# Kernel tuning notes

Hardware: AMD Instinct MI355X
Metric: run time of the kernel (lower is better)

The kernel has to match this reference:

```python
import jax, jax.numpy as jnp
import numpy as np

B, S, DIN = 16, 960, 7
HID, HEADS, LAYERS = 512, 8, 4
PERIODS = (24, 48, 96)
OUT_LEN = 96
HEAD_DIM = HID // HEADS
FFN = 4 * HID


def setup_inputs() -> dict:
    key = jax.random.key(0)
    ks = jax.random.split(key, 20)
    sc = 0.02
    return {
        "x": jax.random.normal(ks[0], (B, S, DIN), dtype=jnp.float32),
        "input_proj_w": jax.random.normal(ks[1], (HID, DIN), dtype=jnp.float32) * sc,
        "input_proj_b": jnp.zeros((HID,), dtype=jnp.float32),
        "in_proj_w": jax.random.normal(ks[2], (LAYERS, 3 * HID, HID), dtype=jnp.float32) * sc,
        "in_proj_b": jnp.zeros((LAYERS, 3 * HID), dtype=jnp.float32),
        "out_proj_w": jax.random.normal(ks[3], (LAYERS, HID, HID), dtype=jnp.float32) * sc,
        "out_proj_b": jnp.zeros((LAYERS, HID), dtype=jnp.float32),
        "ffn_w1": jax.random.normal(ks[4], (LAYERS, FFN, HID), dtype=jnp.float32) * sc,
        "ffn_b1": jnp.zeros((LAYERS, FFN), dtype=jnp.float32),
        "ffn_w2": jax.random.normal(ks[5], (LAYERS, HID, FFN), dtype=jnp.float32) * sc,
        "ffn_b2": jnp.zeros((LAYERS, HID), dtype=jnp.float32),
        "ln1_w": jnp.ones((LAYERS, HID), dtype=jnp.float32),
        "ln1_b": jnp.zeros((LAYERS, HID), dtype=jnp.float32),
        "ln2_w": jnp.ones((LAYERS, HID), dtype=jnp.float32),
        "ln2_b": jnp.zeros((LAYERS, HID), dtype=jnp.float32),
        "output_proj_w": jax.random.normal(ks[6], (1, HID), dtype=jnp.float32) * sc,
        "output_proj_b": jnp.zeros((1,), dtype=jnp.float32),
    }


def _layer_norm(x, w, b, eps=1e-5):
    mu = jnp.mean(x, axis=-1, keepdims=True)
    var = jnp.mean(jnp.square(x - mu), axis=-1, keepdims=True)
    return (x - mu) * jax.lax.rsqrt(var + eps) * w + b


def _mha(x, wqkv, bqkv, wo, bo):
    # x: [N, P, H]; self-attention, PyTorch nn.MultiheadAttention math (eval mode)
    N, P, _ = x.shape
    qkv = x @ wqkv.T + bqkv                      # [N, P, 3H]
    q, k, v = jnp.split(qkv, 3, axis=-1)
    q = q.reshape(N, P, HEADS, HEAD_DIM)
    k = k.reshape(N, P, HEADS, HEAD_DIM)
    v = v.reshape(N, P, HEADS, HEAD_DIM)
    scores = jnp.einsum("nqhd,nkhd->nhqk", q, k) / jnp.sqrt(jnp.float32(HEAD_DIM))
    attn = jax.nn.softmax(scores, axis=-1)
    out = jnp.einsum("nhqk,nkhd->nqhd", attn, v).reshape(N, P, HID)
    return out @ wo.T + bo


def _times_block(x, period, wqkv, bqkv, wo, bo, w1, b1, w2, b2, g1, be1, g2, be2):
    # x: [B, S, H], S % period == 0. Batch all period slices together
    # (replaces the original Python loop over num_periods).
    Bc, Sc, H = x.shape
    xb = x.reshape(Bc * (Sc // period), period, H)
    attn = _mha(xb, wqkv, bqkv, wo, bo)
    xb = _layer_norm(xb + attn, g1, be1)
    ffn = jax.nn.gelu(xb @ w1.T + b1, approximate=False) @ w2.T + b2
    xb = _layer_norm(xb + ffn, g2, be2)
    return xb.reshape(Bc, Sc, H)


def reference(x, input_proj_w, input_proj_b, in_proj_w, in_proj_b, out_proj_w,
              out_proj_b, ffn_w1, ffn_b1, ffn_w2, ffn_b2, ln1_w, ln1_b,
              ln2_w, ln2_b, output_proj_w, output_proj_b):
    h = x @ input_proj_w.T + input_proj_b        # [B, S, H]
    branches = []
    for period in PERIODS:
        ph = h
        for l in range(LAYERS):
            ph = _times_block(ph, period,
                              in_proj_w[l], in_proj_b[l], out_proj_w[l], out_proj_b[l],
                              ffn_w1[l], ffn_b1[l], ffn_w2[l], ffn_b2[l],
                              ln1_w[l], ln1_b[l], ln2_w[l], ln2_b[l])
        branches.append(ph)
    h = jnp.mean(jnp.stack(branches, axis=0), axis=0)     # [B, S, H]
    out = h @ output_proj_w.T + output_proj_b             # [B, S, 1]
    # AdaptiveAvgPool1d(OUT_LEN) with S % OUT_LEN == 0 -> uniform block mean
    out = out.reshape(B, OUT_LEN, S // OUT_LEN, 1).mean(axis=2)  # [B, OUT_LEN, 1]
    return out
```

## Files before the change

### kernel.cpp

```cpp
#include <hip/hip_runtime.h>
#include <hip/hip_bf16.h>

typedef __bf16 bf16;
typedef __attribute__((ext_vector_type(8))) __bf16 bf16x8;
typedef __attribute__((ext_vector_type(4))) __bf16 bf16x4;
typedef __attribute__((ext_vector_type(4))) float f32x4;

#define TOKENS 15360
#define HID    512
#define FFN_D  2048
#define QKV_D  1536

__device__ __forceinline__ float gelu_erf(float x) {
  const float z = fabsf(x) * 0.70710678118654752f;
#if __has_builtin(__builtin_amdgcn_rcpf)
  const float t = __builtin_amdgcn_rcpf(fmaf(0.3275911f, z, 1.f));
#else
  const float t = 1.f / fmaf(0.3275911f, z, 1.f);
#endif
  float p = fmaf(1.061405429f, t, -1.453152027f);
  p = fmaf(p, t, 1.421413741f);
  p = fmaf(p, t, -0.284496736f);
  p = fmaf(p, t, 0.254829592f);
  p *= t;
  const float e  = __expf(-z * z);
  const float er = fmaf(-p, e, 1.f);
  return 0.5f * x * (1.f + copysignf(er, x));
}

__global__ __launch_bounds__(256) void cvt_kernel(const float* __restrict__ src,
                                                  bf16* __restrict__ dst, int n4) {
  const int i = (blockIdx.x * 256 + threadIdx.x);
  if (i >= n4) return;
  const float4 v = ((const float4*)src)[i];
  bf16x4 d = {(bf16)v.x, (bf16)v.y, (bf16)v.z, (bf16)v.w};
  *(bf16x4*)(dst + (size_t)i * 4) = d;
}

__global__ __launch_bounds__(256) void cvt_w2_kernel(const float* __restrict__ src,
                                                     bf16* __restrict__ dst, int n4) {
  const int i = (blockIdx.x * 256 + threadIdx.x);
  if (i >= n4) return;
  const int f  = i * 4;
  const int ln = f >> 11;
  const int c2 = f & 2047;
  const int h  = c2 >> 10;
  const int c  = c2 & 1023;
  const int l  = ln >> 9;
  const int n  = ln & 511;
  const float4 v = ((const float4*)src)[i];
  bf16x4 d = {(bf16)v.x, (bf16)v.y, (bf16)v.z, (bf16)v.w};
  *(bf16x4*)(dst + ((((size_t)(l * 2 + h) * 512 + n) << 10) + c)) = d;
}

#define EPI_BIAS_BF16     0
#define EPI_BIAS_RES_BF16 1
#define EPI_BIAS_GELU     2
#define EPI_RES_BF16      3

template <int EPI>
__global__ __launch_bounds__(256) void gemm_bt(
    const bf16* __restrict__ A, const bf16* __restrict__ W,
    const float* __restrict__ bias, const bf16* __restrict__ R,
    bf16* __restrict__ out, int M, int N, int K) {
  __shared__ __align__(16) bf16 As[2 * 128 * 64];
  __shared__ __align__(16) bf16 Bs[2 * 128 * 64];

  const int tid  = threadIdx.x;
  const int lane = tid & 63;
  const int wv   = tid >> 6;
  const int li   = lane & 15;
  const int qd   = lane >> 4;
  const int mw   = (wv & 1) << 6;
  const int nw   = (wv >> 1) << 6;

  const int NB  = gridDim.x;
  const int nwg = NB * gridDim.y;
  int lid = blockIdx.y * NB + blockIdx.x;
  if ((nwg & 7) == 0) lid = (lid & 7) * (nwg >> 3) + (lid >> 3);
  const int n0 = (lid % NB) << 7;
  const int m0 = (lid / NB) << 7;

  f32x4 acc[4][4];
#pragma unroll
  for (int i = 0; i < 4; ++i)
#pragma unroll
    for (int j = 0; j < 4; ++j) acc[i][j] = (f32x4){0.f, 0.f, 0.f, 0.f};

  const bf16* pa[4];
  const bf16* pb[4];
  int off[4];
#pragma unroll
  for (int it = 0; it < 4; ++it) {
    const int fc   = it * 256 + tid;
    const int r    = fc >> 3;
    const int c    = fc & 7;
    const int koff = (c ^ (r & 7)) << 3;
    pa[it]  = A + (size_t)(m0 + r) * K + koff;
    pb[it]  = W + (size_t)(n0 + r) * K + koff;
    off[it] = (it * 256 + (tid & 192)) * 8;
  }

  auto stage = [&](int buf) {
#pragma unroll
    for (int it = 0; it < 4; ++it) {
      __builtin_amdgcn_global_load_lds(
          (const __attribute__((address_space(1))) unsigned int*)pa[it],
          (__attribute__((address_space(3))) unsigned int*)(As + buf * 8192 + off[it]),
          16, 0, 0);
      pa[it] += 64;
    }
#pragma unroll
    for (int it = 0; it < 4; ++it) {
      __builtin_amdgcn_global_load_lds(
          (const __attribute__((address_space(1))) unsigned int*)pb[it],
          (__attribute__((address_space(3))) unsigned int*)(Bs + buf * 8192 + off[it]),
          16, 0, 0);
      pb[it] += 64;
    }
  };

  auto compute = [&](int buf) {
    const bf16* Ab = As + buf * 8192;
    const bf16* Bb = Bs + buf * 8192;
#pragma unroll
    for (int ks = 0; ks < 2; ++ks) {
      const int ck = (ks << 2) + qd;
      bf16x8 af[4], bfv[4];
#pragma unroll
      for (int i = 0; i < 4; ++i) {
        const int mr = mw + i * 16 + li;
        af[i] = *(const bf16x8*)(Ab + mr * 64 + ((ck ^ (li & 7)) << 3));
      }
#pragma unroll
      for (int j = 0; j < 4; ++j) {
        const int nr = nw + j * 16 + li;
        bfv[j] = *(const bf16x8*)(Bb + nr * 64 + ((ck ^ (li & 7)) << 3));
      }
#pragma unroll
      for (int i = 0; i < 4; ++i)
#pragma unroll
        for (int j = 0; j < 4; ++j)
          acc[i][j] = __builtin_amdgcn_mfma_f32_16x16x32_bf16(af[i], bfv[j],
                                                              acc[i][j], 0, 0, 0);
    }
  };

  stage(0);
  int cur = 0;
  for (int k0 = 0; k0 < K - 64; k0 += 64) {
    stage(cur ^ 1);
    asm volatile("s_waitcnt vmcnt(8)" ::: "memory");
    __builtin_amdgcn_s_barrier();
    asm volatile("" ::: "memory");
    compute(cur);
    asm volatile("" ::: "memory");
    __builtin_amdgcn_s_barrier();
    asm volatile("" ::: "memory");
    cur ^= 1;
  }
  asm volatile("s_waitcnt vmcnt(0)" ::: "memory");
  __builtin_amdgcn_s_barrier();
  asm volatile("" ::: "memory");
  compute(cur);

#pragma unroll
  for (int i = 0; i < 4; ++i) {
    const int mrow = m0 + mw + i * 16 + qd * 4;
#pragma unroll
    for (int j = 0; j < 4; ++j) {
      const int ncol = n0 + nw + j * 16 + li;
      float bv = 0.f;
      if (EPI != EPI_RES_BF16) bv = bias[ncol];
#pragma unroll
      for (int r = 0; r < 4; ++r) {
        const size_t off2 = (size_t)(mrow + r) * N + ncol;
        float v = acc[i][j][r] + bv;
        if (EPI == EPI_BIAS_RES_BF16 || EPI == EPI_RES_BF16) v += (float)R[off2];
        out[off2] = (EPI == EPI_BIAS_GELU) ? (bf16)gelu_erf(v) : (bf16)v;
      }
    }
  }
}

template <int P>
__global__ __launch_bounds__(256) void attn_kernel(const bf16* __restrict__ qkv,
                                                   bf16* __restrict__ out) {
  constexpr int PP   = ((P + 15) / 16) * 16;
  constexpr int PK   = ((PP + 31) / 32) * 32;
  constexpr int MT   = PP / 16;
  constexpr int SSTR = PP + 2;
  constexpr int VSTR = PK + 8;
  constexpr int PSTR = PK + 8;
  constexpr int G    = (P * 8 <= 256) ? 8 : ((P * 4 <= 256) ? 4 : 2);

  __shared__ __align__(16) bf16 QK[2 * PP * 64];
  __shared__ __align__(16) bf16 Vt[64 * VSTR];
  __shared__ __align__(16) float Sm[PP * SSTR];
  __shared__ float rsum[PP];

  bf16* Qs = QK;
  bf16* Ks = QK + PP * 64;
  bf16* Ps = QK;

  const int tid  = threadIdx.x;
  const int lane = tid & 63;
  const int wv   = tid >> 6;
  const int li   = lane & 15;
  const int qd   = lane >> 4;
  const int n    = blockIdx.x >> 3;
  const int h    = blockIdx.x & 7;
  const bf16* base = qkv + (size_t)n * P * QKV_D + h * 64;

  for (int t = tid; t < P * 8; t += 256) {
    const int r = t >> 3, c = t & 7;
    const bf16x8 qv = *(const bf16x8*)(base + (size_t)r * QKV_D + c * 8);
    const bf16x8 kv = *(const bf16x8*)(base + (size_t)r * QKV_D + 512 + c * 8);
    *(bf16x8*)(Qs + r * 64 + ((c ^ (r & 7)) * 8)) = qv;
    *(bf16x8*)(Ks + r * 64 + ((c ^ (r & 7)) * 8)) = kv;
  }
  for (int t = tid; t < P * 8; t += 256) {
    const int j = t % P, dc = t / P;
    const bf16x8 vv = *(const bf16x8*)(base + (size_t)j * QKV_D + 1024 + dc * 8);
#pragma unroll
    for (int u = 0; u < 8; ++u) Vt[(dc * 8 + u) * VSTR + j] = vv[u];
  }
  if constexpr (PK > P) {
    for (int t = tid; t < 64 * (PK - P); t += 256) {
      const int d = t / (PK - P), j = P + t % (PK - P);
      Vt[d * VSTR + j] = (bf16)0.f;
    }
  }
  __syncthreads();

  for (int t = wv; t < MT * MT; t += 4) {
    const int ti = t / MT, tj = t % MT;
    f32x4 acc = (f32x4){0.f, 0.f, 0.f, 0.f};
#pragma unroll
    for (int ks = 0; ks < 2; ++ks) {
      const int ck = ks * 4 + qd;
      const int ar = ti * 16 + li;
      const int br = tj * 16 + li;
      const bf16x8 af = *(const bf16x8*)(Qs + ar * 64 + ((ck ^ (ar & 7)) * 8));
      const bf16x8 bv = *(const bf16x8*)(Ks + br * 64 + ((ck ^ (br & 7)) * 8));
      acc = __builtin_amdgcn_mfma_f32_16x16x32_bf16(af, bv, acc, 0, 0, 0);
    }
#pragma unroll
    for (int r = 0; r < 4; ++r)
      Sm[(ti * 16 + qd * 4 + r) * SSTR + tj * 16 + li] = acc[r];
  }
  __syncthreads();

  if (tid < P * G) {
    const int row = tid / G, g = tid % G;
    const float* srow = Sm + row * SSTR;
    bf16* prow = Ps + row * PSTR;
    float mx = -1e30f;
    for (int j = g; j < P; j += G) mx = fmaxf(mx, srow[j]);
#pragma unroll
    for (int m = G >> 1; m; m >>= 1) mx = fmaxf(mx, __shfl_xor(mx, m, 64));
    mx *= 0.125f;
    float sum = 0.f;
    for (int j = g; j < P; j += G) {
      const float e = __expf(srow[j] * 0.125f - mx);
      sum += e;
      prow[j] = (bf16)e;
    }
#pragma unroll
    for (int m = G >> 1; m; m >>= 1) sum += __shfl_xor(sum, m, 64);
    for (int j = P + g; j < PK; j += G) prow[j] = (bf16)0.f;
    if (g == 0) rsum[row] = 1.f / sum;
  }
  __syncthreads();

  for (int t = wv; t < MT * 4; t += 4) {
    const int ti = t >> 2, td = t & 3;
    f32x4 acc = (f32x4){0.f, 0.f, 0.f, 0.f};
#pragma unroll
    for (int ks = 0; ks < PK / 32; ++ks) {
      const int ck = ks * 4 + qd;
      const bf16x8 af = *(const bf16x8*)(Ps + (ti * 16 + li) * PSTR + ck * 8);
      const bf16x8 bv = *(const bf16x8*)(Vt + (td * 16 + li) * VSTR + ck * 8);
      acc = __builtin_amdgcn_mfma_f32_16x16x32_bf16(af, bv, acc, 0, 0, 0);
    }
#pragma unroll
    for (int r = 0; r < 4; ++r) {
      const int row = ti * 16 + qd * 4 + r;
      if (row < P)
        out[(size_t)(n * P + row) * HID + h * 64 + td * 16 + li] =
            (bf16)(acc[r] * rsum[row]);
    }
  }
}

__global__ __launch_bounds__(256) void ln_kernel(const bf16* __restrict__ Y,
                                                 const float* __restrict__ w,
                                                 const float* __restrict__ b,
                                                 bf16* __restrict__ X) {
  const int row  = blockIdx.x * 4 + (threadIdx.x >> 6);
  const int lane = threadIdx.x & 63;
  const bf16x8 yv = *(const bf16x8*)(Y + (size_t)row * HID + 8 * lane);
  float y[8];
#pragma unroll
  for (int u = 0; u < 8; ++u) y[u] = (float)yv[u];
  float s = 0.f, s2 = 0.f;
#pragma unroll
  for (int u = 0; u < 8; ++u) { s += y[u]; s2 += y[u] * y[u]; }
#pragma unroll
  for (int off = 32; off > 0; off >>= 1) {
    s  += __shfl_xor(s, off, 64);
    s2 += __shfl_xor(s2, off, 64);
  }
  const float mean = s * (1.f / 512.f);
  const float var  = s2 * (1.f / 512.f) - mean * mean;
  const float rstd = rsqrtf(var + 1e-5f);
  const float4 w0 = ((const float4*)w)[2 * lane];
  const float4 w1 = ((const float4*)w)[2 * lane + 1];
  const float4 b0 = ((const float4*)b)[2 * lane];
  const float4 b1 = ((const float4*)b)[2 * lane + 1];
  const float wr[8] = {w0.x, w0.y, w0.z, w0.w, w1.x, w1.y, w1.z, w1.w};
  const float br[8] = {b0.x, b0.y, b0.z, b0.w, b1.x, b1.y, b1.z, b1.w};
  bf16x8 o;
#pragma unroll
  for (int u = 0; u < 8; ++u) o[u] = (bf16)((y[u] - mean) * rstd * wr[u] + br[u]);
  *(bf16x8*)(X + (size_t)row * HID + 8 * lane) = o;
}

__global__ __launch_bounds__(256) void inproj_kernel(const float* __restrict__ x,
                                                     const float* __restrict__ w,
                                                     const float* __restrict__ b,
                                                     bf16* __restrict__ h,
                                                     int nbr) {
  const int idx = blockIdx.x * 256 + threadIdx.x;
  const int r = idx >> 9, o = idx & 511;
  float s = b[o];
#pragma unroll
  for (int k = 0; k < 7; ++k) s += x[r * 7 + k] * w[o * 7 + k];
  const bf16 bv = (bf16)s;
  for (int q = 0; q < nbr; ++q) h[idx + (size_t)q * TOKENS * HID] = bv;
}

__global__ __launch_bounds__(256) void outdot_kernel(const bf16* __restrict__ X,
                                                     const float* __restrict__ w,
                                                     float* __restrict__ acc,
                                                     int first) {
  const int row  = blockIdx.x * 4 + (threadIdx.x >> 6);
  const int lane = threadIdx.x & 63;
  const bf16* xr = X + (size_t)row * HID;
  const bf16x8 xa = *(const bf16x8*)(xr + 8 * lane);
  const float4 wa = ((const float4*)w)[2 * lane];
  const float4 wb = ((const float4*)w)[2 * lane + 1];
  float s = (float)xa[0] * wa.x + (float)xa[1] * wa.y + (float)xa[2] * wa.z +
            (float)xa[3] * wa.w + (float)xa[4] * wb.x + (float)xa[5] * wb.y +
            (float)xa[6] * wb.z + (float)xa[7] * wb.w;
#pragma unroll
  for (int off = 32; off > 0; off >>= 1) s += __shfl_xor(s, off, 64);
  if (lane == 0) acc[row] = first ? s : (acc[row] + s);
}

__global__ __launch_bounds__(256) void pool_kernel(const float* __restrict__ acc,
                                                   const float* __restrict__ ob,
                                                   float* __restrict__ out) {
  const int idx = blockIdx.x * 256 + threadIdx.x;
  if (idx >= 16 * 96) return;
  const int bb = idx / 96, o = idx % 96;
  float s = 0.f;
#pragma unroll
  for (int j = 0; j < 10; ++j) s += acc[bb * 960 + o * 10 + j];
  out[idx] = s * (1.f / 30.f) + ob[0];
}

extern "C" void kernel_launch(void* const* d_in, const int* in_sizes, int n_in,
                              void* d_out, int out_size, void* d_ws,
                              size_t ws_size, hipStream_t stream) {
  const float* x          = (const float*)d_in[0];
  const float* ip_w       = (const float*)d_in[1];
  const float* ip_b       = (const float*)d_in[2];
  const float* in_proj_w  = (const float*)d_in[3];
  const float* in_proj_b  = (const float*)d_in[4];
  const float* out_proj_w = (const float*)d_in[5];
  const float* out_proj_b = (const float*)d_in[6];
  const float* ffn_w1     = (const float*)d_in[7];
  const float* ffn_b1     = (const float*)d_in[8];
  const float* ffn_w2     = (const float*)d_in[9];
  const float* ffn_b2     = (const float*)d_in[10];
  const float* ln1_w      = (const float*)d_in[11];
  const float* ln1_b      = (const float*)d_in[12];
  const float* ln2_w      = (const float*)d_in[13];
  const float* ln2_b      = (const float*)d_in[14];
  const float* op_w       = (const float*)d_in[15];
  const float* op_b       = (const float*)d_in[16];

  char* p = (char*)d_ws;
  bf16* Wq  = (bf16*)p; p += (size_t)4 * QKV_D * HID * 2;
  bf16* Wo  = (bf16*)p; p += (size_t)4 * HID * HID * 2;
  bf16* W1  = (bf16*)p; p += (size_t)4 * FFN_D * HID * 2;
  bf16* W2s = (bf16*)p; p += (size_t)4 * HID * FFN_D * 2;
  float* ACC = (float*)p; p += (size_t)TOKENS * 4;
  const size_t remain = ws_size - (size_t)(p - (char*)d_ws);

  const size_t T3 = 3 * (size_t)TOKENS;
  const size_t need_batched = T3 * HID * 2 + T3 * (size_t)FFN_D * 2;
  const size_t need_seq =
      (size_t)TOKENS * HID * 2 + (size_t)TOKENS * FFN_D * 2;
  const bool batched = remain >= need_batched;
  if (!batched && remain < need_seq) return;

  {
    const int nq = 4 * QKV_D * HID / 4, no = 4 * HID * HID / 4,
              n1 = 4 * FFN_D * HID / 4, n2 = 4 * HID * FFN_D / 4;
    cvt_kernel<<<(nq + 255) / 256, 256, 0, stream>>>(in_proj_w, Wq, nq);
    cvt_kernel<<<(no + 255) / 256, 256, 0, stream>>>(out_proj_w, Wo, no);
    cvt_kernel<<<(n1 + 255) / 256, 256, 0, stream>>>(ffn_w1, W1, n1);
    cvt_w2_kernel<<<(n2 + 255) / 256, 256, 0, stream>>>(ffn_w2, W2s, n2);
  }

  static const int periods[3] = {24, 48, 96};
  auto launch_attn = [&](int P, const bf16* q, bf16* o) {
    const int nblk = (TOKENS / P) * 8;
    if (P == 24)      attn_kernel<24><<<nblk, 256, 0, stream>>>(q, o);
    else if (P == 48) attn_kernel<48><<<nblk, 256, 0, stream>>>(q, o);
    else              attn_kernel<96><<<nblk, 256, 0, stream>>>(q, o);
  };

  auto run_layer = [&](int l, int M, bf16* X, bf16* QKV, bf16* ATT, bf16* YB,
                       bf16* H, bool all_br, int br) {
    const int MB = M / 128;
    gemm_bt<EPI_BIAS_BF16><<<dim3(QKV_D / 128, MB), 256, 0, stream>>>(
        X, Wq + (size_t)l * QKV_D * HID, in_proj_b + l * QKV_D, nullptr,
        QKV, M, QKV_D, HID);
    if (all_br) {
      for (int b2 = 0; b2 < 3; ++b2)
        launch_attn(periods[b2], QKV + (size_t)b2 * TOKENS * QKV_D,
                    ATT + (size_t)b2 * TOKENS * HID);
    } else {
      launch_attn(periods[br], QKV, ATT);
    }
    gemm_bt<EPI_BIAS_RES_BF16><<<dim3(HID / 128, MB), 256, 0, stream>>>(
        ATT, Wo + (size_t)l * HID * HID, out_proj_b + l * HID, X, YB,
        M, HID, HID);
    ln_kernel<<<M / 4, 256, 0, stream>>>(YB, ln1_w + l * HID, ln1_b + l * HID, X);
    gemm_bt<EPI_BIAS_GELU><<<dim3(1024 / 128, MB), 256, 0, stream>>>(
        X, W1 + (size_t)l * FFN_D * HID, ffn_b1 + l * FFN_D, nullptr,
        H, M, 1024, HID);
    gemm_bt<EPI_BIAS_RES_BF16><<<dim3(HID / 128, MB), 256, 0, stream>>>(
        H, W2s + (size_t)(l * 2 + 0) * HID * 1024, ffn_b2 + l * HID, X, YB,
        M, HID, 1024);
    gemm_bt<EPI_BIAS_GELU><<<dim3(1024 / 128, MB), 256, 0, stream>>>(
        X, W1 + (size_t)l * FFN_D * HID + (size_t)1024 * HID,
        ffn_b1 + l * FFN_D + 1024, nullptr, H, M, 1024, HID);
    gemm_bt<EPI_RES_BF16><<<dim3(HID / 128, MB), 256, 0, stream>>>(
        H, W2s + (size_t)(l * 2 + 1) * HID * 1024, nullptr, YB, YB,
        M, HID, 1024);
    ln_kernel<<<M / 4, 256, 0, stream>>>(YB, ln2_w + l * HID, ln2_b + l * HID, X);
  };

  if (batched) {
    bf16* X   = (bf16*)p; p += T3 * HID * 2;
    bf16* BUF = (bf16*)p;
    bf16* QKV = BUF;
    bf16* ATT = BUF + T3 * QKV_D;
    bf16* H   = BUF;
    bf16* YB  = BUF + T3 * 1024;
    const int M = (int)T3;

    inproj_kernel<<<TOKENS * HID / 256, 256, 0, stream>>>(x, ip_w, ip_b, X, 3);
    for (int l = 0; l < 4; ++l)
      run_layer(l, M, X, QKV, ATT, YB, H, true, 0);
    for (int br = 0; br < 3; ++br)
      outdot_kernel<<<TOKENS / 4, 256, 0, stream>>>(
          X + (size_t)br * TOKENS * HID, op_w, ACC, br == 0);
  } else {
    bf16* X   = (bf16*)p; p += (size_t)TOKENS * HID * 2;
    bf16* SCR = (bf16*)p; p += (size_t)TOKENS * FFN_D * 2;
    bf16* QKV = SCR;
    bf16* ATT = SCR + (size_t)TOKENS * QKV_D;
    bf16* H   = SCR;
    bf16* YB  = SCR + (size_t)TOKENS * 1024;
    const int M = TOKENS;

    for (int br = 0; br < 3; ++br) {
      inproj_kernel<<<TOKENS * HID / 256, 256, 0, stream>>>(x, ip_w, ip_b, X, 1);
      for (int l = 0; l < 4; ++l)
        run_layer(l, M, X, QKV, ATT, YB, H, false, br);
      outdot_kernel<<<TOKENS / 4, 256, 0, stream>>>(X, op_w, ACC, br == 0);
    }
  }
  pool_kernel<<<6, 256, 0, stream>>>(ACC, op_b, (float*)d_out);
}
```

Before: 2.203 ms.

## Share layer-0 QKV across branches and unsplit FFN when workspace allows

At layer 0 all three period branches start from the same input projection, so the QKV GEMM now runs once on TOKENS rows and every branch's attention reads that shared result. When the workspace is large enough, the FFN becomes one full-width GELU GEMM and one K=2048 down-projection. This replaces the two half-width pairs, removing extra launches and a residual round-trip through YB. The unsplit path needs a separate YB buffer and so more workspace. It also converts W2 without the split layout.

```diff
diff --git a/kernel.cpp b/kernel.cpp
--- a/kernel.cpp
+++ b/kernel.cpp
@@ -392,18 +392,19 @@
   const float* op_b       = (const float*)d_in[16];
 
   char* p = (char*)d_ws;
-  bf16* Wq  = (bf16*)p; p += (size_t)4 * QKV_D * HID * 2;
-  bf16* Wo  = (bf16*)p; p += (size_t)4 * HID * HID * 2;
-  bf16* W1  = (bf16*)p; p += (size_t)4 * FFN_D * HID * 2;
-  bf16* W2s = (bf16*)p; p += (size_t)4 * HID * FFN_D * 2;
+  bf16* Wq = (bf16*)p; p += (size_t)4 * QKV_D * HID * 2;
+  bf16* Wo = (bf16*)p; p += (size_t)4 * HID * HID * 2;
+  bf16* W1 = (bf16*)p; p += (size_t)4 * FFN_D * HID * 2;
+  bf16* W2 = (bf16*)p; p += (size_t)4 * HID * FFN_D * 2;
   float* ACC = (float*)p; p += (size_t)TOKENS * 4;
   const size_t remain = ws_size - (size_t)(p - (char*)d_ws);
 
   const size_t T3 = 3 * (size_t)TOKENS;
-  const size_t need_batched = T3 * HID * 2 + T3 * (size_t)FFN_D * 2;
-  const size_t need_seq =
-      (size_t)TOKENS * HID * 2 + (size_t)TOKENS * FFN_D * 2;
-  const bool batched = remain >= need_batched;
+  const size_t need_unsplit = T3 * HID * 2 + T3 * (size_t)FFN_D * 2 + T3 * HID * 2;
+  const size_t need_split   = T3 * HID * 2 + T3 * (size_t)FFN_D * 2;
+  const size_t need_seq     = (size_t)TOKENS * HID * 2 + (size_t)TOKENS * FFN_D * 2;
+  const bool unsplit = remain >= need_unsplit;
+  const bool batched = remain >= need_split;
   if (!batched && remain < need_seq) return;
 
   {
@@ -412,7 +413,10 @@
     cvt_kernel<<<(nq + 255) / 256, 256, 0, stream>>>(in_proj_w, Wq, nq);
     cvt_kernel<<<(no + 255) / 256, 256, 0, stream>>>(out_proj_w, Wo, no);
     cvt_kernel<<<(n1 + 255) / 256, 256, 0, stream>>>(ffn_w1, W1, n1);
-    cvt_w2_kernel<<<(n2 + 255) / 256, 256, 0, stream>>>(ffn_w2, W2s, n2);
+    if (unsplit)
+      cvt_kernel<<<(n2 + 255) / 256, 256, 0, stream>>>(ffn_w2, W2, n2);
+    else
+      cvt_w2_kernel<<<(n2 + 255) / 256, 256, 0, stream>>>(ffn_w2, W2, n2);
   }
 
   static const int periods[3] = {24, 48, 96};
@@ -423,16 +427,17 @@
     else              attn_kernel<96><<<nblk, 256, 0, stream>>>(q, o);
   };
 
-  auto run_layer = [&](int l, int M, bf16* X, bf16* QKV, bf16* ATT, bf16* YB,
-                       bf16* H, bool all_br, int br) {
+  auto run_layer = [&](int l, int M, int qkvM, bf16* X, bf16* QKV, bf16* ATT,
+                       bf16* YB, bf16* H, bool all_br, int br, bool unspl) {
     const int MB = M / 128;
-    gemm_bt<EPI_BIAS_BF16><<<dim3(QKV_D / 128, MB), 256, 0, stream>>>(
+    gemm_bt<EPI_BIAS_BF16><<<dim3(QKV_D / 128, qkvM / 128), 256, 0, stream>>>(
         X, Wq + (size_t)l * QKV_D * HID, in_proj_b + l * QKV_D, nullptr,
-        QKV, M, QKV_D, HID);
+        QKV, qkvM, QKV_D, HID);
     if (all_br) {
-      for (int b2 = 0; b2 < 3; ++b2)
-        launch_attn(periods[b2], QKV + (size_t)b2 * TOKENS * QKV_D,
-                    ATT + (size_t)b2 * TOKENS * HID);
+      for (int b2 = 0; b2 < 3; ++b2) {
+        const bf16* q = QKV + (qkvM == M ? (size_t)b2 * TOKENS * QKV_D : 0);
+        launch_attn(periods[b2], q, ATT + (size_t)b2 * TOKENS * HID);
+      }
     } else {
       launch_attn(periods[br], QKV, ATT);
     }
@@ -440,33 +445,48 @@
         ATT, Wo + (size_t)l * HID * HID, out_proj_b + l * HID, X, YB,
         M, HID, HID);
     ln_kernel<<<M / 4, 256, 0, stream>>>(YB, ln1_w + l * HID, ln1_b + l * HID, X);
-    gemm_bt<EPI_BIAS_GELU><<<dim3(1024 / 128, MB), 256, 0, stream>>>(
-        X, W1 + (size_t)l * FFN_D * HID, ffn_b1 + l * FFN_D, nullptr,
-        H, M, 1024, HID);
-    gemm_bt<EPI_BIAS_RES_BF16><<<dim3(HID / 128, MB), 256, 0, stream>>>(
-        H, W2s + (size_t)(l * 2 + 0) * HID * 1024, ffn_b2 + l * HID, X, YB,
-        M, HID, 1024);
-    gemm_bt<EPI_BIAS_GELU><<<dim3(1024 / 128, MB), 256, 0, stream>>>(
-        X, W1 + (size_t)l * FFN_D * HID + (size_t)1024 * HID,
-        ffn_b1 + l * FFN_D + 1024, nullptr, H, M, 1024, HID);
-    gemm_bt<EPI_RES_BF16><<<dim3(HID / 128, MB), 256, 0, stream>>>(
-        H, W2s + (size_t)(l * 2 + 1) * HID * 1024, nullptr, YB, YB,
-        M, HID, 1024);
+    if (unspl) {
+      gemm_bt<EPI_BIAS_GELU><<<dim3(FFN_D / 128, MB), 256, 0, stream>>>(
+          X, W1 + (size_t)l * FFN_D * HID, ffn_b1 + l * FFN_D, nullptr,
+          H, M, FFN_D, HID);
+      gemm_bt<EPI_BIAS_RES_BF16><<<dim3(HID / 128, MB), 256, 0, stream>>>(
+          H, W2 + (size_t)l * HID * FFN_D, ffn_b2 + l * HID, X, YB,
+          M, HID, FFN_D);
+    } else {
+      gemm_bt<EPI_BIAS_GELU><<<dim3(1024 / 128, MB), 256, 0, stream>>>(
+          X, W1 + (size_t)l * FFN_D * HID, ffn_b1 + l * FFN_D, nullptr,
+          H, M, 1024, HID);
+      gemm_bt<EPI_BIAS_RES_BF16><<<dim3(HID / 128, MB), 256, 0, stream>>>(
+          H, W2 + (size_t)(l * 2 + 0) * HID * 1024, ffn_b2 + l * HID, X, YB,
+          M, HID, 1024);
+      gemm_bt<EPI_BIAS_GELU><<<dim3(1024 / 128, MB), 256, 0, stream>>>(
+          X, W1 + (size_t)l * FFN_D * HID + (size_t)1024 * HID,
+          ffn_b1 + l * FFN_D + 1024, nullptr, H, M, 1024, HID);
+      gemm_bt<EPI_RES_BF16><<<dim3(HID / 128, MB), 256, 0, stream>>>(
+          H, W2 + (size_t)(l * 2 + 1) * HID * 1024, nullptr, YB, YB,
+          M, HID, 1024);
+    }
     ln_kernel<<<M / 4, 256, 0, stream>>>(YB, ln2_w + l * HID, ln2_b + l * HID, X);
   };
 
   if (batched) {
     bf16* X   = (bf16*)p; p += T3 * HID * 2;
-    bf16* BUF = (bf16*)p;
+    bf16* BUF = (bf16*)p; p += T3 * (size_t)FFN_D * 2;
     bf16* QKV = BUF;
     bf16* ATT = BUF + T3 * QKV_D;
-    bf16* H   = BUF;
-    bf16* YB  = BUF + T3 * 1024;
+    bf16* H, * YB;
+    if (unsplit) {
+      H  = BUF;
+      YB = (bf16*)p;
+    } else {
+      H  = BUF;
+      YB = BUF + T3 * 1024;
+    }
     const int M = (int)T3;
 
     inproj_kernel<<<TOKENS * HID / 256, 256, 0, stream>>>(x, ip_w, ip_b, X, 3);
     for (int l = 0; l < 4; ++l)
-      run_layer(l, M, X, QKV, ATT, YB, H, true, 0);
+      run_layer(l, M, l == 0 ? TOKENS : M, X, QKV, ATT, YB, H, true, 0, unsplit);
     for (int br = 0; br < 3; ++br)
       outdot_kernel<<<TOKENS / 4, 256, 0, stream>>>(
           X + (size_t)br * TOKENS * HID, op_w, ACC, br == 0);
@@ -482,7 +502,7 @@
     for (int br = 0; br < 3; ++br) {
       inproj_kernel<<<TOKENS * HID / 256, 256, 0, stream>>>(x, ip_w, ip_b, X, 1);
       for (int l = 0; l < 4; ++l)
-        run_layer(l, M, X, QKV, ATT, YB, H, false, br);
+        run_layer(l, M, M, X, QKV, ATT, YB, H, false, br, false);
       outdot_kernel<<<TOKENS / 4, 256, 0, stream>>>(X, op_w, ACC, br == 0);
     }
   }
```

Result: no change. 2.214 ms (+0.5%).
